# Kernel tuning notes

Measured on AMD Instinct MI355X. Metric: run time of the kernel, lower is better.

Reference implementation:

```python
import jax, jax.numpy as jnp
import numpy as np

B_, L_, H_, P_ = 8, 4096, 512, 256
DT_LO, DT_HI = 1e-3, 4e-3  # keep Heinsen log-space weights in fp32 range for L=4096


def setup_inputs() -> dict:
    key = jax.random.key(0)
    ks = jax.random.split(key, 8)
    u = jax.random.normal(ks[0], (B_, L_, H_), dtype=jnp.float32)
    # Diagonal continuous-time state matrix Lambda (HiPPO-N-like: Re=-0.5, structured imag parts)
    lambda_re = -0.5 * jnp.ones((P_,), dtype=jnp.float32)
    lambda_im = jnp.pi * (jnp.arange(P_, dtype=jnp.float32) + 1.0)
    # Input/output projections (complex, stored as re/im pairs)
    B_re = jax.random.normal(ks[1], (P_, H_), dtype=jnp.float32) / jnp.sqrt(float(H_))
    B_im = jax.random.normal(ks[2], (P_, H_), dtype=jnp.float32) / jnp.sqrt(float(H_))
    C_re = jax.random.normal(ks[3], (H_, P_), dtype=jnp.float32) / jnp.sqrt(float(P_))
    C_im = jax.random.normal(ks[4], (H_, P_), dtype=jnp.float32) / jnp.sqrt(float(P_))
    D = jax.random.normal(ks[5], (H_,), dtype=jnp.float32)
    # Per-state learnable log-timescales, log-uniform in [DT_LO, DT_HI]
    log_delta = jax.random.uniform(ks[6], (P_,), dtype=jnp.float32,
                                   minval=jnp.log(DT_LO), maxval=jnp.log(DT_HI))
    return {"u": u, "lambda_re": lambda_re, "lambda_im": lambda_im,
            "B_re": B_re, "B_im": B_im, "C_re": C_re, "C_im": C_im,
            "D": D, "log_delta": log_delta}


def reference(u, lambda_re, lambda_im, B_re, B_im, C_re, C_im, D, log_delta):
    # --- ZOH discretization (eq. 6 of S5 paper) ---
    lam = lambda_re + 1j * lambda_im                     # (P,) complex64
    delta = jnp.exp(log_delta)                           # (P,)
    lambda_bar = jnp.exp(lam * delta)                    # (P,) complex
    B_tilde = B_re + 1j * B_im                           # (P,H)
    B_bar = ((lambda_bar - 1.0) / lam)[:, None] * B_tilde  # (P,H)

    # --- input projection: Bu_k = B_bar @ u_k ---
    Bu = jnp.einsum('blh,ph->blp', u.astype(B_bar.dtype), B_bar)  # (B,L,P) complex

    # --- Heinsen log-space parallel scan: x_k = lambda_bar * x_{k-1} + Bu_k ---
    L = u.shape[1]
    log_lambda = jnp.log(lambda_bar)                     # (P,) complex
    k = jnp.arange(L, dtype=jnp.float32)
    weights = jnp.exp(k[:, None] * log_lambda[None, :])  # (L,P) complex
    xs = weights[None] * jnp.cumsum(Bu / weights[None], axis=1)  # (B,L,P)

    # --- output: y_k = 2*Re(C_tilde x_k) + D*u_k (conjugate symmetry) ---
    C_tilde = C_re + 1j * C_im                           # (H,P)
    y = 2.0 * jnp.real(jnp.einsum('blp,hp->blh', xs, C_tilde)) + D * u
    return y
```

## Files before the change

### kernel.cpp

```cpp
#include <hip/hip_runtime.h>
#include <hip/hip_bf16.h>
#include <math.h>

#define HH 512
#define PP 256
#define LSEQ 4096
#define BB 8
#define MTOT (BB*LSEQ)
#define N2P 512

typedef __attribute__((ext_vector_type(8))) short bf16x8;
typedef __attribute__((ext_vector_type(4))) float f32x4;
typedef __attribute__((ext_vector_type(8))) unsigned short u16x8;
typedef __attribute__((ext_vector_type(4))) unsigned short u16x4;

#define SWZ(row) (((((row) & 7) ^ (((row) >> 3) & 7)) << 4))

__device__ inline unsigned short f2b(float x) {
    return __builtin_bit_cast(unsigned short, __float2bfloat16(x));
}
__device__ inline float b2f(unsigned short h) {
    union { unsigned int u; float f; } v; v.u = ((unsigned int)h) << 16;
    return v.f;
}

#define GLOAD16(gp, lp) __builtin_amdgcn_global_load_lds( \
    (const __attribute__((address_space(1))) unsigned int*)(gp), \
    (__attribute__((address_space(3))) unsigned int*)(lp), 16, 0, 0)

__device__ inline size_t panel_off(int r, int k) {
    int nblk = r >> 7, rl = r & 127;
    int kblk = k >> 6, kl = k & 63;
    int c = kl >> 3, j = kl & 7;
    return (size_t)(nblk * 8 + kblk) * 16384 + rl * 128 + ((c * 16) ^ SWZ(rl)) + j * 2;
}

__global__ void prep_w1_k(const float* __restrict__ lre, const float* __restrict__ lim,
                          const float* __restrict__ logd,
                          const float* __restrict__ Bre, const float* __restrict__ Bim,
                          char* __restrict__ W1s, float2* __restrict__ lamb) {
    int idx = blockIdx.x * 256 + threadIdx.x;
    if (idx >= PP * HH) return;
    int p = idx >> 9;
    int h = idx & (HH - 1);
    float delta = expf(logd[p]);
    float lr = lre[p], li = lim[p];
    float er = expf(lr * delta);
    float th = li * delta;
    float lbr = er * cosf(th), lbi = er * sinf(th);
    if (h == 0) lamb[p] = make_float2(lbr, lbi);
    float a = lbr - 1.0f, b = lbi;
    float n2 = lr * lr + li * li;
    float gr = (a * lr + b * li) / n2;
    float gi = (b * lr - a * li) / n2;
    float br = Bre[idx], bi = Bim[idx];
    *(unsigned short*)(W1s + panel_off(p, h))      = f2b(gr * br - gi * bi);
    *(unsigned short*)(W1s + panel_off(PP + p, h)) = f2b(gr * bi + gi * br);
}

__global__ void prep_w2_k(const float* __restrict__ Cre, const float* __restrict__ Cim,
                          char* __restrict__ W2s) {
    int idx = blockIdx.x * 256 + threadIdx.x;
    if (idx >= HH * N2P) return;
    int h = idx >> 9;
    int k = idx & 511;
    float v = (k < PP) ? 2.0f * Cre[(size_t)h * PP + k]
                       : -2.0f * Cim[(size_t)h * PP + (k - PP)];
    *(unsigned short*)(W2s + panel_off(h, k)) = f2b(v);
}

#define TILE_COMPUTE(ABUF, BBUF) { \
    bf16x8 af[4][2], bfr[4][2]; \
    _Pragma("unroll") for (int f = 0; f < 4; ++f) { \
      _Pragma("unroll") for (int kk = 0; kk < 2; ++kk) { \
        int ar = wm + f * 16 + (lane & 15); \
        af[f][kk]  = *(const bf16x8*)((ABUF) + ar * 128 + ((kk * 64 + (lane >> 4) * 16) ^ SWZ(ar))); \
        int br = wn + f * 16 + (lane & 15); \
        bfr[f][kk] = *(const bf16x8*)((BBUF) + br * 128 + ((kk * 64 + (lane >> 4) * 16) ^ SWZ(br))); } } \
    _Pragma("unroll") for (int fm = 0; fm < 4; ++fm) { \
      _Pragma("unroll") for (int fn = 0; fn < 4; ++fn) { \
        _Pragma("unroll") for (int kk = 0; kk < 2; ++kk) { \
          acc[fm][fn] = __builtin_amdgcn_mfma_f32_16x16x32_bf16(af[fm][kk], bfr[fn][kk], acc[fm][fn], 0, 0, 0); } } } }

__global__ __launch_bounds__(256) void gemm1_k(const float* __restrict__ u,
                                               const char* __restrict__ W1s,
                                               unsigned short* __restrict__ T1) {
    __shared__ char smem[65536];
    const int tid = threadIdx.x, wave = tid >> 6, lane = tid & 63;
    const int swz = (blockIdx.x & 7) * 128 + (blockIdx.x >> 3);
    const int m0 = (swz >> 2) * 128;
    const int nblk = swz & 3, n0 = nblk * 128;
    const int wm = (wave >> 1) * 64, wn = (wave & 1) * 64;
    const int arow = tid >> 3, acol = tid & 7;

    float4 av0[4], av1[4];
    f32x4 acc[4][4] = {};

#define G1_A_LOAD(K0) { \
    _Pragma("unroll") for (int it = 0; it < 4; ++it) { \
        int row = it * 32 + arow; \
        const float* src = &u[(size_t)(m0 + row) * HH + (K0) + acol * 8]; \
        av0[it] = *(const float4*)src; av1[it] = *(const float4*)(src + 4); } }

#define G1_A_WRITE(ABUF) { \
    _Pragma("unroll") for (int it = 0; it < 4; ++it) { \
        int row = it * 32 + arow; \
        bf16x8 pk; \
        pk[0] = (short)f2b(av0[it].x); pk[1] = (short)f2b(av0[it].y); \
        pk[2] = (short)f2b(av0[it].z); pk[3] = (short)f2b(av0[it].w); \
        pk[4] = (short)f2b(av1[it].x); pk[5] = (short)f2b(av1[it].y); \
        pk[6] = (short)f2b(av1[it].z); pk[7] = (short)f2b(av1[it].w); \
        *(bf16x8*)((ABUF) + row * 128 + ((acol * 16) ^ SWZ(row))) = pk; } }

#define G1_B_GLOAD(K0, BBUF) { \
    const char* panel = W1s + (size_t)(nblk * 8 + ((K0) >> 6)) * 16384 + wave * 4096 + lane * 16; \
    _Pragma("unroll") for (int q = 0; q < 4; ++q) \
        GLOAD16(panel + q * 1024, (BBUF) + wave * 4096 + q * 1024); }

    char* A0 = smem;          char* B0 = smem + 16384;
    char* A1 = smem + 32768;  char* B1 = smem + 49152;

    G1_A_LOAD(0); G1_B_GLOAD(0, B0); G1_A_WRITE(A0);
    asm volatile("s_waitcnt vmcnt(0)" ::: "memory");
    __syncthreads();

    #pragma unroll
    for (int t = 0; t < 8; ++t) {
        char* Ac = (t & 1) ? A1 : A0; char* Bc = (t & 1) ? B1 : B0;
        char* An = (t & 1) ? A0 : A1; char* Bn = (t & 1) ? B0 : B1;
        if (t < 7) { G1_A_LOAD((t + 1) * 64); G1_B_GLOAD((t + 1) * 64, Bn); }
        TILE_COMPUTE(Ac, Bc);
        if (t < 7) { G1_A_WRITE(An); }
        asm volatile("s_waitcnt vmcnt(0)" ::: "memory");
        __syncthreads();
    }

    #pragma unroll
    for (int fm = 0; fm < 4; ++fm) {
        #pragma unroll
        for (int fn = 0; fn < 4; ++fn) {
            int r = n0 + wn + fn * 16 + (lane & 15);
            int m = m0 + wm + fm * 16 + ((lane >> 4) << 2);
            u16x4 pk;
            pk[0] = f2b(acc[fm][fn][0]); pk[1] = f2b(acc[fm][fn][1]);
            pk[2] = f2b(acc[fm][fn][2]); pk[3] = f2b(acc[fm][fn][3]);
            *(u16x4*)&T1[(size_t)r * MTOT + m] = pk;
        }
    }
}

__global__ __launch_bounds__(256) void gemm2_k(const unsigned short* __restrict__ Xs,
                                               const char* __restrict__ W2s,
                                               float* __restrict__ y,
                                               const float* __restrict__ u,
                                               const float* __restrict__ D) {
    __shared__ char smem[65536];
    const int tid = threadIdx.x, wave = tid >> 6, lane = tid & 63;
    const int swz = (blockIdx.x & 7) * 128 + (blockIdx.x >> 3);
    const int m0 = (swz >> 2) * 128;
    const int nblk = swz & 3, n0 = nblk * 128;
    const int wm = (wave >> 1) * 64, wn = (wave & 1) * 64;
    const int kg = tid >> 4, mc = tid & 15;

    u16x8 xv[4];
    f32x4 acc[4][4] = {};

#define G2_A_LOAD(K0) { \
    _Pragma("unroll") for (int kk = 0; kk < 4; ++kk) \
        xv[kk] = *(const u16x8*)&Xs[(size_t)((K0) + kg * 4 + kk) * MTOT + m0 + mc * 8]; }

#define G2_A_WRITE(ABUF) { \
    _Pragma("unroll") for (int j = 0; j < 8; ++j) { \
        int row = mc * 8 + j; \
        u16x4 o; o[0] = xv[0][j]; o[1] = xv[1][j]; o[2] = xv[2][j]; o[3] = xv[3][j]; \
        *(u16x4*)((ABUF) + row * 128 + ((kg * 8) ^ SWZ(row))) = o; } }

#define G2_B_GLOAD(K0, BBUF) { \
    const char* panel = W2s + (size_t)(nblk * 8 + ((K0) >> 6)) * 16384 + wave * 4096 + lane * 16; \
    _Pragma("unroll") for (int q = 0; q < 4; ++q) \
        GLOAD16(panel + q * 1024, (BBUF) + wave * 4096 + q * 1024); }

    char* A0 = smem;          char* B0 = smem + 16384;
    char* A1 = smem + 32768;  char* B1 = smem + 49152;

    G2_A_LOAD(0); G2_B_GLOAD(0, B0); G2_A_WRITE(A0);
    asm volatile("s_waitcnt vmcnt(0)" ::: "memory");
    __syncthreads();

    #pragma unroll
    for (int t = 0; t < 8; ++t) {
        char* Ac = (t & 1) ? A1 : A0; char* Bc = (t & 1) ? B1 : B0;
        char* An = (t & 1) ? A0 : A1; char* Bn = (t & 1) ? B0 : B1;
        if (t < 7) { G2_A_LOAD((t + 1) * 64); G2_B_GLOAD((t + 1) * 64, Bn); }
        TILE_COMPUTE(Ac, Bc);
        if (t < 7) { G2_A_WRITE(An); }
        asm volatile("s_waitcnt vmcnt(0)" ::: "memory");
        __syncthreads();
    }

    float* epi = (float*)smem;
    float* myepi = epi + wave * 4096;
    #pragma unroll
    for (int fm = 0; fm < 4; ++fm) {
        #pragma unroll
        for (int fn = 0; fn < 4; ++fn) {
            int ml = fm * 16 + ((lane >> 4) << 2);
            int hl = fn * 16 + (lane & 15);
            #pragma unroll
            for (int i = 0; i < 4; ++i)
                myepi[(ml + i) * 64 + hl] = acc[fm][fn][i];
        }
    }
    __syncthreads();

    #pragma unroll
    for (int it = 0; it < 16; ++it) {
        int idx = it * 256 + tid;
        int ml = idx >> 5, c = idx & 31;
        int w = ((ml >> 6) << 1) + (c >> 4);
        const float4 v = *(const float4*)(epi + w * 4096 + (ml & 63) * 64 + (c & 15) * 4);
        int grow = m0 + ml, gcol = n0 + c * 4;
        const float4 uv = *(const float4*)&u[(size_t)grow * HH + gcol];
        const float4 dv = *(const float4*)&D[gcol];
        float4 o = make_float4(v.x + dv.x * uv.x, v.y + dv.y * uv.y,
                               v.z + dv.z * uv.z, v.w + dv.w * uv.w);
        *(float4*)&y[(size_t)grow * HH + gcol] = o;
    }
}

__global__ __launch_bounds__(256) void scan_k(const unsigned short* __restrict__ T1,
                                              unsigned short* __restrict__ Xs,
                                              const float2* __restrict__ lamb) {
    const int b = blockIdx.x >> 8;
    const int p = blockIdx.x & 255;
    const int t = threadIdx.x;
    const float2 L = lamb[p];

    const size_t baseRe = (size_t)p * MTOT + (size_t)b * LSEQ + t * 16;
    const size_t baseIm = (size_t)(PP + p) * MTOT + (size_t)b * LSEQ + t * 16;

    u16x8 r0 = *(const u16x8*)&T1[baseRe];
    u16x8 r1 = *(const u16x8*)&T1[baseRe + 8];
    u16x8 i0 = *(const u16x8*)&T1[baseIm];
    u16x8 i1 = *(const u16x8*)&T1[baseIm + 8];

    float re[16], im[16];
    #pragma unroll
    for (int j = 0; j < 8; ++j) {
        re[j] = b2f(r0[j]); re[8 + j] = b2f(r1[j]);
        im[j] = b2f(i0[j]); im[8 + j] = b2f(i1[j]);
    }

    float sr = 0.f, si = 0.f;
    #pragma unroll
    for (int j = 0; j < 16; ++j) {
        float nsr = L.x * sr - L.y * si + re[j];
        si = L.x * si + L.y * sr + im[j];
        sr = nsr;
    }

    __shared__ float cr[256], ci[256];
    cr[t] = sr; ci[t] = si;
    __syncthreads();

    float wr = L.x, wi = L.y;
    #pragma unroll
    for (int q = 0; q < 4; ++q) { float nr = wr * wr - wi * wi; wi = 2.f * wr * wi; wr = nr; }

    for (int off = 1; off < 256; off <<= 1) {
        float pr = 0.f, pi = 0.f;
        const bool has = (t >= off);
        if (has) { pr = cr[t - off]; pi = ci[t - off]; }
        __syncthreads();
        if (has) {
            sr += wr * pr - wi * pi;
            si += wr * pi + wi * pr;
            cr[t] = sr; ci[t] = si;
        }
        __syncthreads();
        float nr = wr * wr - wi * wi; wi = 2.f * wr * wi; wr = nr;
    }

    float xr = 0.f, xi = 0.f;
    if (t > 0) { xr = cr[t - 1]; xi = ci[t - 1]; }

    u16x8 o0, o1, o2, o3;
    #pragma unroll
    for (int j = 0; j < 16; ++j) {
        float nr = L.x * xr - L.y * xi + re[j];
        xi = L.x * xi + L.y * xr + im[j];
        xr = nr;
        if (j < 8) { o0[j] = f2b(xr); o2[j] = f2b(xi); }
        else       { o1[j - 8] = f2b(xr); o3[j - 8] = f2b(xi); }
    }
    *(u16x8*)&Xs[baseRe]     = o0;
    *(u16x8*)&Xs[baseRe + 8] = o1;
    *(u16x8*)&Xs[baseIm]     = o2;
    *(u16x8*)&Xs[baseIm + 8] = o3;
}


extern "C" void kernel_launch(void* const* d_in, const int* in_sizes, int n_in,
                              void* d_out, int out_size, void* d_ws, size_t ws_size,
                              hipStream_t stream) {
    const float* u    = (const float*)d_in[0];
    const float* lre  = (const float*)d_in[1];
    const float* lim  = (const float*)d_in[2];
    const float* Bre  = (const float*)d_in[3];
    const float* Bim  = (const float*)d_in[4];
    const float* Cre  = (const float*)d_in[5];
    const float* Cim  = (const float*)d_in[6];
    const float* Dv   = (const float*)d_in[7];
    const float* logd = (const float*)d_in[8];
    float* out = (float*)d_out;

    char* ws = (char*)d_ws;
    char*           W1s  = ws;
    char*           W2s  = ws + (512 << 10);
    float2*         lamb = (float2*)(ws + (1 << 20));
    unsigned short* Xs   = (unsigned short*)(ws + (1 << 20) + 4096);

    unsigned short* T1 = (unsigned short*)d_out;

    prep_w1_k<<<(PP * HH) / 256, 256, 0, stream>>>(lre, lim, logd, Bre, Bim, W1s, lamb);
    prep_w2_k<<<(HH * N2P) / 256, 256, 0, stream>>>(Cre, Cim, W2s);

    gemm1_k<<<1024, 256, 0, stream>>>(u, W1s, T1);
    scan_k<<<BB * PP, 256, 0, stream>>>(T1, Xs, lamb);
    gemm2_k<<<1024, 256, 0, stream>>>(Xs, W2s, out, u, Dv);
}
```

Before: 97.63 us.

## Pre-convert u to swizzled bf16 panels and retile gemm1 to 256x256 blocks

Adds a separate conversion kernel that writes u as bf16 in the pre-swizzled panel layout, so gemm1 can stage both operands with direct global-to-LDS loads. gemm1 moves from 128x128 tiles with 256 threads to 256x256 tiles with 512 threads and 128KB LDS, issuing MFMAs in quarter-tile phases with raised wave priority. The aim is higher operand reuse and less in-loop VALU conversion. The cost is an extra kernel launch, an extra write and read of a 32MB bf16 copy of u, many added barriers per k-step, and fewer blocks in the grid.

```diff
diff --git a/kernel.cpp b/kernel.cpp
--- a/kernel.cpp
+++ b/kernel.cpp
@@ -69,6 +69,122 @@
     *(unsigned short*)(W2s + panel_off(h, k)) = f2b(v);
 }
 
+__global__ __launch_bounds__(256) void conv_k(const float* __restrict__ u,
+                                              char* __restrict__ ub) {
+    const int tid = threadIdx.x;
+    const int mblk = blockIdx.x >> 2;
+    const int sub = blockIdx.x & 3;
+    const int ml = sub * 32 + (tid >> 3);
+    const int kt = tid & 7;
+    const float* src = &u[(size_t)(mblk * 128 + ml) * HH + kt * 64];
+    char* dst = ub + ((size_t)(mblk * 8 + kt)) * 16384 + ml * 128;
+    #pragma unroll
+    for (int c = 0; c < 8; ++c) {
+        float4 v0 = *(const float4*)(src + c * 8);
+        float4 v1 = *(const float4*)(src + c * 8 + 4);
+        bf16x8 pk;
+        pk[0] = (short)f2b(v0.x); pk[1] = (short)f2b(v0.y);
+        pk[2] = (short)f2b(v0.z); pk[3] = (short)f2b(v0.w);
+        pk[4] = (short)f2b(v1.x); pk[5] = (short)f2b(v1.y);
+        pk[6] = (short)f2b(v1.z); pk[7] = (short)f2b(v1.w);
+        *(bf16x8*)(dst + ((c * 16) ^ SWZ(ml))) = pk;
+    }
+}
+
+
+#define STAGE(GSRC, LDST) { \
+    const char* _s = (GSRC) + wave * 1024 + lane * 16; \
+    char* _d = (LDST) + wave * 1024 + lane * 16; \
+    GLOAD16(_s, _d); GLOAD16(_s + 8192, _d + 8192); }
+
+#define READ_FRAGS(AS, BS, MH, NH) { \
+    _Pragma("unroll") for (int f = 0; f < 4; ++f) { \
+      int ar = wm + (MH) * 64 + f * 16 + (lane & 15); \
+      _Pragma("unroll") for (int kk = 0; kk < 2; ++kk) \
+        af[f][kk] = *(const bf16x8*)((AS) + ar * 128 + ((kk * 64 + (lane >> 4) * 16) ^ SWZ(ar))); } \
+    _Pragma("unroll") for (int g = 0; g < 2; ++g) { \
+      int br = wn + (NH) * 32 + g * 16 + (lane & 15); \
+      _Pragma("unroll") for (int kk = 0; kk < 2; ++kk) \
+        bfv[g][kk] = *(const bf16x8*)((BS) + br * 128 + ((kk * 64 + (lane >> 4) * 16) ^ SWZ(br))); } }
+
+#define MFMA16(MH, NH) { \
+    __builtin_amdgcn_s_setprio(1); \
+    _Pragma("unroll") for (int f = 0; f < 4; ++f) \
+      _Pragma("unroll") for (int g = 0; g < 2; ++g) \
+        _Pragma("unroll") for (int kk = 0; kk < 2; ++kk) \
+          acc[(MH) * 4 + f][(NH) * 2 + g] = __builtin_amdgcn_mfma_f32_16x16x32_bf16( \
+              af[f][kk], bfv[g][kk], acc[(MH) * 4 + f][(NH) * 2 + g], 0, 0, 0); \
+    __builtin_amdgcn_s_setprio(0); }
+
+__global__ __launch_bounds__(512, 2) void gemm1_k(const char* __restrict__ ub,
+                                                  const char* __restrict__ W1s,
+                                                  unsigned short* __restrict__ T1) {
+    __shared__ char smem[131072];
+    const int tid = threadIdx.x, wave = tid >> 6, lane = tid & 63;
+    const int bx = blockIdx.x, by = blockIdx.y;
+    const int m0 = by * 256, n0 = bx * 256;
+    const int wm = (wave >> 2) * 128, wn = (wave & 3) * 64;
+
+    f32x4 acc[8][4] = {};
+    bf16x8 af[4][2], bfv[2][2];
+
+    STAGE(ub  + ((size_t)((by * 2 + 0) * 8 + 0)) * 16384, smem + 0);
+    STAGE(ub  + ((size_t)((by * 2 + 1) * 8 + 0)) * 16384, smem + 16384);
+    STAGE(W1s + ((size_t)((bx * 2 + 0) * 8 + 0)) * 16384, smem + 32768);
+    STAGE(W1s + ((size_t)((bx * 2 + 1) * 8 + 0)) * 16384, smem + 49152);
+
+    for (int t = 0; t < 7; ++t) {
+        char* As = smem + (t & 1) * 65536;
+        char* Bs = As + 32768;
+        char* An = smem + ((t + 1) & 1) * 65536;
+        char* Bn = An + 32768;
+        STAGE(ub + ((size_t)((by * 2 + 0) * 8 + (t + 1))) * 16384, An);
+        STAGE(ub + ((size_t)((by * 2 + 1) * 8 + (t + 1))) * 16384, An + 16384);
+        asm volatile("s_waitcnt vmcnt(4)" ::: "memory");
+        __syncthreads();
+        READ_FRAGS(As, Bs, 0, 0);
+        MFMA16(0, 0);
+        __syncthreads();
+        READ_FRAGS(As, Bs, 1, 0);
+        STAGE(W1s + ((size_t)((bx * 2 + 0) * 8 + (t + 1))) * 16384, Bn);
+        STAGE(W1s + ((size_t)((bx * 2 + 1) * 8 + (t + 1))) * 16384, Bn + 16384);
+        __syncthreads();
+        MFMA16(1, 0);
+        __syncthreads();
+        READ_FRAGS(As, Bs, 0, 1);
+        __syncthreads();
+        MFMA16(0, 1);
+        __syncthreads();
+        READ_FRAGS(As, Bs, 1, 1);
+        __syncthreads();
+        MFMA16(1, 1);
+        __syncthreads();
+    }
+    {
+        char* As = smem + 65536;
+        char* Bs = As + 32768;
+        asm volatile("s_waitcnt vmcnt(0)" ::: "memory");
+        __syncthreads();
+        READ_FRAGS(As, Bs, 0, 0); MFMA16(0, 0);
+        READ_FRAGS(As, Bs, 1, 0); MFMA16(1, 0);
+        READ_FRAGS(As, Bs, 0, 1); MFMA16(0, 1);
+        READ_FRAGS(As, Bs, 1, 1); MFMA16(1, 1);
+    }
+
+    #pragma unroll
+    for (int fm = 0; fm < 8; ++fm) {
+        #pragma unroll
+        for (int fn = 0; fn < 4; ++fn) {
+            int r = n0 + wn + fn * 16 + (lane & 15);
+            int m = m0 + wm + fm * 16 + ((lane >> 4) << 2);
+            u16x4 pk;
+            pk[0] = f2b(acc[fm][fn][0]); pk[1] = f2b(acc[fm][fn][1]);
+            pk[2] = f2b(acc[fm][fn][2]); pk[3] = f2b(acc[fm][fn][3]);
+            *(u16x4*)&T1[(size_t)r * MTOT + m] = pk;
+        }
+    }
+}
+
 #define TILE_COMPUTE(ABUF, BBUF) { \
     bf16x8 af[4][2], bfr[4][2]; \
     _Pragma("unroll") for (int f = 0; f < 4; ++f) { \
@@ -81,73 +197,6 @@
       _Pragma("unroll") for (int fn = 0; fn < 4; ++fn) { \
         _Pragma("unroll") for (int kk = 0; kk < 2; ++kk) { \
           acc[fm][fn] = __builtin_amdgcn_mfma_f32_16x16x32_bf16(af[fm][kk], bfr[fn][kk], acc[fm][fn], 0, 0, 0); } } } }
-
-__global__ __launch_bounds__(256) void gemm1_k(const float* __restrict__ u,
-                                               const char* __restrict__ W1s,
-                                               unsigned short* __restrict__ T1) {
-    __shared__ char smem[65536];
-    const int tid = threadIdx.x, wave = tid >> 6, lane = tid & 63;
-    const int swz = (blockIdx.x & 7) * 128 + (blockIdx.x >> 3);
-    const int m0 = (swz >> 2) * 128;
-    const int nblk = swz & 3, n0 = nblk * 128;
-    const int wm = (wave >> 1) * 64, wn = (wave & 1) * 64;
-    const int arow = tid >> 3, acol = tid & 7;
-
-    float4 av0[4], av1[4];
-    f32x4 acc[4][4] = {};
-
-#define G1_A_LOAD(K0) { \
-    _Pragma("unroll") for (int it = 0; it < 4; ++it) { \
-        int row = it * 32 + arow; \
-        const float* src = &u[(size_t)(m0 + row) * HH + (K0) + acol * 8]; \
-        av0[it] = *(const float4*)src; av1[it] = *(const float4*)(src + 4); } }
-
-#define G1_A_WRITE(ABUF) { \
-    _Pragma("unroll") for (int it = 0; it < 4; ++it) { \
-        int row = it * 32 + arow; \
-        bf16x8 pk; \
-        pk[0] = (short)f2b(av0[it].x); pk[1] = (short)f2b(av0[it].y); \
-        pk[2] = (short)f2b(av0[it].z); pk[3] = (short)f2b(av0[it].w); \
-        pk[4] = (short)f2b(av1[it].x); pk[5] = (short)f2b(av1[it].y); \
-        pk[6] = (short)f2b(av1[it].z); pk[7] = (short)f2b(av1[it].w); \
-        *(bf16x8*)((ABUF) + row * 128 + ((acol * 16) ^ SWZ(row))) = pk; } }
-
-#define G1_B_GLOAD(K0, BBUF) { \
-    const char* panel = W1s + (size_t)(nblk * 8 + ((K0) >> 6)) * 16384 + wave * 4096 + lane * 16; \
-    _Pragma("unroll") for (int q = 0; q < 4; ++q) \
-        GLOAD16(panel + q * 1024, (BBUF) + wave * 4096 + q * 1024); }
-
-    char* A0 = smem;          char* B0 = smem + 16384;
-    char* A1 = smem + 32768;  char* B1 = smem + 49152;
-
-    G1_A_LOAD(0); G1_B_GLOAD(0, B0); G1_A_WRITE(A0);
-    asm volatile("s_waitcnt vmcnt(0)" ::: "memory");
-    __syncthreads();
-
-    #pragma unroll
-    for (int t = 0; t < 8; ++t) {
-        char* Ac = (t & 1) ? A1 : A0; char* Bc = (t & 1) ? B1 : B0;
-        char* An = (t & 1) ? A0 : A1; char* Bn = (t & 1) ? B0 : B1;
-        if (t < 7) { G1_A_LOAD((t + 1) * 64); G1_B_GLOAD((t + 1) * 64, Bn); }
-        TILE_COMPUTE(Ac, Bc);
-        if (t < 7) { G1_A_WRITE(An); }
-        asm volatile("s_waitcnt vmcnt(0)" ::: "memory");
-        __syncthreads();
-    }
-
-    #pragma unroll
-    for (int fm = 0; fm < 4; ++fm) {
-        #pragma unroll
-        for (int fn = 0; fn < 4; ++fn) {
-            int r = n0 + wn + fn * 16 + (lane & 15);
-            int m = m0 + wm + fm * 16 + ((lane >> 4) << 2);
-            u16x4 pk;
-            pk[0] = f2b(acc[fm][fn][0]); pk[1] = f2b(acc[fm][fn][1]);
-            pk[2] = f2b(acc[fm][fn][2]); pk[3] = f2b(acc[fm][fn][3]);
-            *(u16x4*)&T1[(size_t)r * MTOT + m] = pk;
-        }
-    }
-}
 
 __global__ __launch_bounds__(256) void gemm2_k(const unsigned short* __restrict__ Xs,
                                                const char* __restrict__ W2s,
@@ -319,13 +368,15 @@
     char*           W2s  = ws + (512 << 10);
     float2*         lamb = (float2*)(ws + (1 << 20));
     unsigned short* Xs   = (unsigned short*)(ws + (1 << 20) + 4096);
+    char*           ubp  = ws + (1 << 20) + 4096 + ((size_t)32 << 20);
 
     unsigned short* T1 = (unsigned short*)d_out;
 
     prep_w1_k<<<(PP * HH) / 256, 256, 0, stream>>>(lre, lim, logd, Bre, Bim, W1s, lamb);
     prep_w2_k<<<(HH * N2P) / 256, 256, 0, stream>>>(Cre, Cim, W2s);
 
-    gemm1_k<<<1024, 256, 0, stream>>>(u, W1s, T1);
+    conv_k<<<1024, 256, 0, stream>>>(u, ubp);
+    gemm1_k<<<dim3(2, 128), 512, 0, stream>>>(ubp, W1s, T1);
     scan_k<<<BB * PP, 256, 0, stream>>>(T1, Xs, lamb);
     gemm2_k<<<1024, 256, 0, stream>>>(Xs, W2s, out, u, Dv);
 }
```

Result: slower. 126.5 us (+29.6%).

## Use 8 waves per GEMM block with 64x32 wave tiles

Applied to the files above, without the earlier changes.

Both GEMM kernels move from 256 to 512 threads per block, so each wave computes a 64x32 tile instead of 64x64. The accumulator register footprint per wave halves, and launch bounds request 4 blocks/SM worth of occupancy. Global load and LDS write mappings and the epilogue staging are rewritten for the new thread count, and the main K loop is no longer force-unrolled. Per-wave A-fragment reuse drops, so LDS read traffic per MFMA rises.

```diff
diff --git a/kernel.cpp b/kernel.cpp
--- a/kernel.cpp
+++ b/kernel.cpp
@@ -70,65 +70,68 @@
 }
 
 #define TILE_COMPUTE(ABUF, BBUF) { \
-    bf16x8 af[4][2], bfr[4][2]; \
+    bf16x8 af[4][2], bfv[2][2]; \
     _Pragma("unroll") for (int f = 0; f < 4; ++f) { \
-      _Pragma("unroll") for (int kk = 0; kk < 2; ++kk) { \
-        int ar = wm + f * 16 + (lane & 15); \
-        af[f][kk]  = *(const bf16x8*)((ABUF) + ar * 128 + ((kk * 64 + (lane >> 4) * 16) ^ SWZ(ar))); \
-        int br = wn + f * 16 + (lane & 15); \
-        bfr[f][kk] = *(const bf16x8*)((BBUF) + br * 128 + ((kk * 64 + (lane >> 4) * 16) ^ SWZ(br))); } } \
-    _Pragma("unroll") for (int fm = 0; fm < 4; ++fm) { \
-      _Pragma("unroll") for (int fn = 0; fn < 4; ++fn) { \
-        _Pragma("unroll") for (int kk = 0; kk < 2; ++kk) { \
-          acc[fm][fn] = __builtin_amdgcn_mfma_f32_16x16x32_bf16(af[fm][kk], bfr[fn][kk], acc[fm][fn], 0, 0, 0); } } } }
-
-__global__ __launch_bounds__(256) void gemm1_k(const float* __restrict__ u,
-                                               const char* __restrict__ W1s,
-                                               unsigned short* __restrict__ T1) {
+      int ar = wm + f * 16 + (lane & 15); \
+      _Pragma("unroll") for (int kk = 0; kk < 2; ++kk) \
+        af[f][kk] = *(const bf16x8*)((ABUF) + ar * 128 + ((kk * 64 + (lane >> 4) * 16) ^ SWZ(ar))); } \
+    _Pragma("unroll") for (int g = 0; g < 2; ++g) { \
+      int br = wn + g * 16 + (lane & 15); \
+      _Pragma("unroll") for (int kk = 0; kk < 2; ++kk) \
+        bfv[g][kk] = *(const bf16x8*)((BBUF) + br * 128 + ((kk * 64 + (lane >> 4) * 16) ^ SWZ(br))); } \
+    _Pragma("unroll") for (int f = 0; f < 4; ++f) \
+      _Pragma("unroll") for (int g = 0; g < 2; ++g) \
+        _Pragma("unroll") for (int kk = 0; kk < 2; ++kk) \
+          acc[f][g] = __builtin_amdgcn_mfma_f32_16x16x32_bf16(af[f][kk], bfv[g][kk], acc[f][g], 0, 0, 0); }
+
+__global__ __launch_bounds__(512, 4) void gemm1_k(const float* __restrict__ u,
+                                                  const char* __restrict__ W1s,
+                                                  unsigned short* __restrict__ T1) {
     __shared__ char smem[65536];
     const int tid = threadIdx.x, wave = tid >> 6, lane = tid & 63;
     const int swz = (blockIdx.x & 7) * 128 + (blockIdx.x >> 3);
     const int m0 = (swz >> 2) * 128;
     const int nblk = swz & 3, n0 = nblk * 128;
-    const int wm = (wave >> 1) * 64, wn = (wave & 1) * 64;
-    const int arow = tid >> 3, acol = tid & 7;
-
-    float4 av0[4], av1[4];
-    f32x4 acc[4][4] = {};
+    const int wm = (wave >> 2) * 64, wn = (wave & 3) * 32;
+    const int arow = tid >> 2, acol = tid & 3;
+
+    float4 av[4];
+    f32x4 acc[4][2] = {};
 
 #define G1_A_LOAD(K0) { \
-    _Pragma("unroll") for (int it = 0; it < 4; ++it) { \
-        int row = it * 32 + arow; \
-        const float* src = &u[(size_t)(m0 + row) * HH + (K0) + acol * 8]; \
-        av0[it] = *(const float4*)src; av1[it] = *(const float4*)(src + 4); } }
+    const float* src = &u[(size_t)(m0 + arow) * HH + (K0) + acol * 16]; \
+    av[0] = *(const float4*)src;       av[1] = *(const float4*)(src + 4); \
+    av[2] = *(const float4*)(src + 8); av[3] = *(const float4*)(src + 12); }
 
 #define G1_A_WRITE(ABUF) { \
-    _Pragma("unroll") for (int it = 0; it < 4; ++it) { \
-        int row = it * 32 + arow; \
-        bf16x8 pk; \
-        pk[0] = (short)f2b(av0[it].x); pk[1] = (short)f2b(av0[it].y); \
-        pk[2] = (short)f2b(av0[it].z); pk[3] = (short)f2b(av0[it].w); \
-        pk[4] = (short)f2b(av1[it].x); pk[5] = (short)f2b(av1[it].y); \
-        pk[6] = (short)f2b(av1[it].z); pk[7] = (short)f2b(av1[it].w); \
-        *(bf16x8*)((ABUF) + row * 128 + ((acol * 16) ^ SWZ(row))) = pk; } }
+    bf16x8 p0, p1; \
+    p0[0] = (short)f2b(av[0].x); p0[1] = (short)f2b(av[0].y); \
+    p0[2] = (short)f2b(av[0].z); p0[3] = (short)f2b(av[0].w); \
+    p0[4] = (short)f2b(av[1].x); p0[5] = (short)f2b(av[1].y); \
+    p0[6] = (short)f2b(av[1].z); p0[7] = (short)f2b(av[1].w); \
+    p1[0] = (short)f2b(av[2].x); p1[1] = (short)f2b(av[2].y); \
+    p1[2] = (short)f2b(av[2].z); p1[3] = (short)f2b(av[2].w); \
+    p1[4] = (short)f2b(av[3].x); p1[5] = (short)f2b(av[3].y); \
+    p1[6] = (short)f2b(av[3].z); p1[7] = (short)f2b(av[3].w); \
+    *(bf16x8*)((ABUF) + arow * 128 + ((acol * 32)      ^ SWZ(arow))) = p0; \
+    *(bf16x8*)((ABUF) + arow * 128 + ((acol * 32 + 16) ^ SWZ(arow))) = p1; }
 
 #define G1_B_GLOAD(K0, BBUF) { \
-    const char* panel = W1s + (size_t)(nblk * 8 + ((K0) >> 6)) * 16384 + wave * 4096 + lane * 16; \
-    _Pragma("unroll") for (int q = 0; q < 4; ++q) \
-        GLOAD16(panel + q * 1024, (BBUF) + wave * 4096 + q * 1024); }
+    const char* pan = W1s + (size_t)(nblk * 8 + ((K0) >> 6)) * 16384 + tid * 16; \
+    GLOAD16(pan, (BBUF) + tid * 16); \
+    GLOAD16(pan + 8192, (BBUF) + tid * 16 + 8192); }
 
     char* A0 = smem;          char* B0 = smem + 16384;
     char* A1 = smem + 32768;  char* B1 = smem + 49152;
 
-    G1_A_LOAD(0); G1_B_GLOAD(0, B0); G1_A_WRITE(A0);
+    G1_B_GLOAD(0, B0); G1_A_LOAD(0); G1_A_WRITE(A0);
     asm volatile("s_waitcnt vmcnt(0)" ::: "memory");
     __syncthreads();
 
-    #pragma unroll
     for (int t = 0; t < 8; ++t) {
         char* Ac = (t & 1) ? A1 : A0; char* Bc = (t & 1) ? B1 : B0;
         char* An = (t & 1) ? A0 : A1; char* Bn = (t & 1) ? B0 : B1;
-        if (t < 7) { G1_A_LOAD((t + 1) * 64); G1_B_GLOAD((t + 1) * 64, Bn); }
+        if (t < 7) { G1_B_GLOAD((t + 1) * 64, Bn); G1_A_LOAD((t + 1) * 64); }
         TILE_COMPUTE(Ac, Bc);
         if (t < 7) { G1_A_WRITE(An); }
         asm volatile("s_waitcnt vmcnt(0)" ::: "memory");
@@ -136,62 +139,62 @@
     }
 
     #pragma unroll
-    for (int fm = 0; fm < 4; ++fm) {
+    for (int f = 0; f < 4; ++f) {
         #pragma unroll
-        for (int fn = 0; fn < 4; ++fn) {
-            int r = n0 + wn + fn * 16 + (lane & 15);
-            int m = m0 + wm + fm * 16 + ((lane >> 4) << 2);
+        for (int g = 0; g < 2; ++g) {
+            int r = n0 + wn + g * 16 + (lane & 15);
+            int m = m0 + wm + f * 16 + ((lane >> 4) << 2);
             u16x4 pk;
-            pk[0] = f2b(acc[fm][fn][0]); pk[1] = f2b(acc[fm][fn][1]);
-            pk[2] = f2b(acc[fm][fn][2]); pk[3] = f2b(acc[fm][fn][3]);
+            pk[0] = f2b(acc[f][g][0]); pk[1] = f2b(acc[f][g][1]);
+            pk[2] = f2b(acc[f][g][2]); pk[3] = f2b(acc[f][g][3]);
             *(u16x4*)&T1[(size_t)r * MTOT + m] = pk;
         }
     }
 }
 
-__global__ __launch_bounds__(256) void gemm2_k(const unsigned short* __restrict__ Xs,
-                                               const char* __restrict__ W2s,
-                                               float* __restrict__ y,
-                                               const float* __restrict__ u,
-                                               const float* __restrict__ D) {
+__global__ __launch_bounds__(512, 4) void gemm2_k(const unsigned short* __restrict__ Xs,
+                                                  const char* __restrict__ W2s,
+                                                  float* __restrict__ y,
+                                                  const float* __restrict__ u,
+                                                  const float* __restrict__ D) {
     __shared__ char smem[65536];
     const int tid = threadIdx.x, wave = tid >> 6, lane = tid & 63;
     const int swz = (blockIdx.x & 7) * 128 + (blockIdx.x >> 3);
     const int m0 = (swz >> 2) * 128;
     const int nblk = swz & 3, n0 = nblk * 128;
-    const int wm = (wave >> 1) * 64, wn = (wave & 1) * 64;
-    const int kg = tid >> 4, mc = tid & 15;
-
-    u16x8 xv[4];
-    f32x4 acc[4][4] = {};
+    const int wm = (wave >> 2) * 64, wn = (wave & 3) * 32;
+    const int kr = tid >> 5;
+    const int mc4 = tid & 31;
+
+    u16x4 xv[4];
+    f32x4 acc[4][2] = {};
 
 #define G2_A_LOAD(K0) { \
     _Pragma("unroll") for (int kk = 0; kk < 4; ++kk) \
-        xv[kk] = *(const u16x8*)&Xs[(size_t)((K0) + kg * 4 + kk) * MTOT + m0 + mc * 8]; }
+        xv[kk] = *(const u16x4*)&Xs[(size_t)((K0) + kr * 4 + kk) * MTOT + m0 + mc4 * 4]; }
 
 #define G2_A_WRITE(ABUF) { \
-    _Pragma("unroll") for (int j = 0; j < 8; ++j) { \
-        int row = mc * 8 + j; \
+    _Pragma("unroll") for (int j = 0; j < 4; ++j) { \
+        int m = mc4 * 4 + j; \
         u16x4 o; o[0] = xv[0][j]; o[1] = xv[1][j]; o[2] = xv[2][j]; o[3] = xv[3][j]; \
-        *(u16x4*)((ABUF) + row * 128 + ((kg * 8) ^ SWZ(row))) = o; } }
+        *(u16x4*)((ABUF) + m * 128 + ((kr * 8) ^ SWZ(m))) = o; } }
 
 #define G2_B_GLOAD(K0, BBUF) { \
-    const char* panel = W2s + (size_t)(nblk * 8 + ((K0) >> 6)) * 16384 + wave * 4096 + lane * 16; \
-    _Pragma("unroll") for (int q = 0; q < 4; ++q) \
-        GLOAD16(panel + q * 1024, (BBUF) + wave * 4096 + q * 1024); }
+    const char* pan = W2s + (size_t)(nblk * 8 + ((K0) >> 6)) * 16384 + tid * 16; \
+    GLOAD16(pan, (BBUF) + tid * 16); \
+    GLOAD16(pan + 8192, (BBUF) + tid * 16 + 8192); }
 
     char* A0 = smem;          char* B0 = smem + 16384;
     char* A1 = smem + 32768;  char* B1 = smem + 49152;
 
-    G2_A_LOAD(0); G2_B_GLOAD(0, B0); G2_A_WRITE(A0);
+    G2_B_GLOAD(0, B0); G2_A_LOAD(0); G2_A_WRITE(A0);
     asm volatile("s_waitcnt vmcnt(0)" ::: "memory");
     __syncthreads();
 
-    #pragma unroll
     for (int t = 0; t < 8; ++t) {
         char* Ac = (t & 1) ? A1 : A0; char* Bc = (t & 1) ? B1 : B0;
         char* An = (t & 1) ? A0 : A1; char* Bn = (t & 1) ? B0 : B1;
-        if (t < 7) { G2_A_LOAD((t + 1) * 64); G2_B_GLOAD((t + 1) * 64, Bn); }
+        if (t < 7) { G2_B_GLOAD((t + 1) * 64, Bn); G2_A_LOAD((t + 1) * 64); }
         TILE_COMPUTE(Ac, Bc);
         if (t < 7) { G2_A_WRITE(An); }
         asm volatile("s_waitcnt vmcnt(0)" ::: "memory");
@@ -199,26 +202,26 @@
     }
 
     float* epi = (float*)smem;
-    float* myepi = epi + wave * 4096;
-    #pragma unroll
-    for (int fm = 0; fm < 4; ++fm) {
+    float* myepi = epi + wave * 2048;
+    #pragma unroll
+    for (int f = 0; f < 4; ++f) {
         #pragma unroll
-        for (int fn = 0; fn < 4; ++fn) {
-            int ml = fm * 16 + ((lane >> 4) << 2);
-            int hl = fn * 16 + (lane & 15);
+        for (int g = 0; g < 2; ++g) {
+            int ml = f * 16 + ((lane >> 4) << 2);
+            int hl = g * 16 + (lane & 15);
             #pragma unroll
             for (int i = 0; i < 4; ++i)
-                myepi[(ml + i) * 64 + hl] = acc[fm][fn][i];
+                myepi[(ml + i) * 32 + hl] = acc[f][g][i];
         }
     }
     __syncthreads();
 
     #pragma unroll
-    for (int it = 0; it < 16; ++it) {
-        int idx = it * 256 + tid;
+    for (int it = 0; it < 8; ++it) {
+        int idx = it * 512 + tid;
         int ml = idx >> 5, c = idx & 31;
-        int w = ((ml >> 6) << 1) + (c >> 4);
-        const float4 v = *(const float4*)(epi + w * 4096 + (ml & 63) * 64 + (c & 15) * 4);
+        int w = ((ml >> 6) << 2) + (c >> 3);
+        const float4 v = *(const float4*)(epi + w * 2048 + (ml & 63) * 32 + (c & 7) * 4);
         int grow = m0 + ml, gcol = n0 + c * 4;
         const float4 uv = *(const float4*)&u[(size_t)grow * HH + gcol];
         const float4 dv = *(const float4*)&D[gcol];
@@ -325,7 +328,7 @@
     prep_w1_k<<<(PP * HH) / 256, 256, 0, stream>>>(lre, lim, logd, Bre, Bim, W1s, lamb);
     prep_w2_k<<<(HH * N2P) / 256, 256, 0, stream>>>(Cre, Cim, W2s);
 
-    gemm1_k<<<1024, 256, 0, stream>>>(u, W1s, T1);
+    gemm1_k<<<1024, 512, 0, stream>>>(u, W1s, T1);
     scan_k<<<BB * PP, 256, 0, stream>>>(T1, Xs, lamb);
-    gemm2_k<<<1024, 256, 0, stream>>>(Xs, W2s, out, u, Dv);
-}
+    gemm2_k<<<1024, 512, 0, stream>>>(Xs, W2s, out, u, Dv);
+}
```

Measured after the change: 104.5 us. 7.0% more time.
